# Performance work log

Hardware: AMD Instinct MI355X
Metric: run time of the kernel (lower is better)

The kernel has to match this reference:

```python
import jax, jax.numpy as jnp
import numpy as np

T_SCALES = [0.0, 0.25, 0.5, 0.75, 1.0]  # ODEblock time_scales; Euler step per consecutive pair
NUM_ZEROS = 10
BETA = 0.6  # defined in ODEFunc but unused in its forward


def _odefunc(x, x0, adj, alpha, w, d, w2, d2):
    # x: [B, N, T, Fa]; adj: [N, N]; alpha: [N]; w: [Fa, Fa]; d: [Fa]; w2: [T, T]; d2: [T]
    a = jax.nn.sigmoid(alpha)[None, :, None, None]              # [1, N, 1, 1]
    xa = jnp.einsum('ij,kjln->kiln', adj, x)                    # adjacency propagation over nodes
    dc = jnp.clip(d, 0.0, 1.0)
    W = (w * dc) @ w.T                                          # [Fa, Fa]
    # NOTE: faithful to torch source: 'ijkl,mn->ijkm' has NO shared contraction
    # index => xw = (sum_l x) outer (sum_n W) — reproduced exactly.
    xw = jnp.einsum('ijkl,mn->ijkm', x, W)
    d2c = jnp.clip(d2, 0.0, 1.0)
    W2 = (w2 * d2c) @ w2.T                                      # [T, T]
    xw2 = jnp.einsum('ijkl,kn->ijnl', x, W2)                    # temporal mixing
    # f = alpha/2*xa - x + xw - x + xw2 - x + x0
    return a * 0.5 * xa - 3.0 * x + xw + xw2 + x0


def setup_inputs() -> dict:
    key = jax.random.key(0)
    k1, k2 = jax.random.split(key)
    B, N, T, F = 32, 512, 24, 64
    Fa = F + NUM_ZEROS
    x = jax.random.normal(k1, (B, N, T, F), dtype=jnp.float32)
    adj = jax.random.uniform(k2, (N, N), dtype=jnp.float32) / N  # normalized dense adjacency
    alpha = 0.8 * jnp.ones((N,), jnp.float32)                    # nn.Parameter init 0.8*ones
    w = jnp.eye(Fa, dtype=jnp.float32)                           # nn.Parameter init eye
    d = jnp.ones((Fa,), jnp.float32)                             # nn.Parameter init ones
    w2 = jnp.eye(T, dtype=jnp.float32)
    d2 = jnp.ones((T,), jnp.float32)
    return {"x": x, "adj": adj, "alpha": alpha, "w": w, "d": d, "w2": w2, "d2": d2}


def reference(x, adj, alpha, w, d, w2, d2):
    B, N, T, F = x.shape
    if F == 64:
        x_aug = jnp.concatenate(
            [x, jnp.zeros((B, N, T, NUM_ZEROS), dtype=x.dtype)], axis=3)
    else:
        x_aug = x
    x0 = jax.lax.stop_gradient(x_aug)  # set_x0 uses clone().detach()
    # Euler odeint with two time points does one step: z = x + dt * f(x).
    # Original loop restarts from x_aug each iteration, so f is constant.
    f = _odefunc(x_aug, x0, adj, alpha, w, d, w2, d2)
    z = x_aug
    for i in range(len(T_SCALES) - 1):
        dt = T_SCALES[i + 1] - T_SCALES[i]
        z = x_aug + dt * f  # overwrites z each iteration, as in the torch code
    return jax.nn.relu(z)
```

## Files before the change

### kernel.cpp

```cpp
#include <hip/hip_runtime.h>
#include <hip/hip_fp16.h>
#include <cstdint>
#include <cstddef>

#define B_  32
#define N_  512
#define T_  24
#define F_  64
#define FA_ 74
#define NC  1536

typedef __attribute__((ext_vector_type(8))) _Float16 half8;
typedef __attribute__((ext_vector_type(8))) unsigned short ushort8;
typedef __attribute__((ext_vector_type(4))) float floatx4;

#define WS_ADJ 1536
#define WS_XT  132608
#define WS_S   12715520

#define AS1(p) ((const __attribute__((address_space(1))) void*)(p))
#define AS3(p) ((__attribute__((address_space(3))) void*)(p))

union h2u { _Float16 h; unsigned short u; };

__global__ __launch_bounds__(256) void prep_kernel(
    const float* __restrict__ x, const float* __restrict__ adj,
    const float* __restrict__ alpha, const float* __restrict__ w,
    const float* __restrict__ d, const float* __restrict__ w2,
    const float* __restrict__ d2, float* __restrict__ ws) {
  __shared__ float tile[64 * 65];
  __shared__ float cs[FA_];
  int bid = blockIdx.x;
  int tid = threadIdx.x;
  if (bid < 6144) {
    _Float16* xT = (_Float16*)(ws + WS_XT);
    float* Sp = ws + WS_S;
    int ct = bid % 24;
    int kt = (bid / 24) % 8;
    int b = bid / 192;
    int c0 = ct * 64;
    int k0 = kt * 64;
#pragma unroll
    for (int it = 0; it < 4; ++it) {
      int g = it * 256 + tid;
      int k = g >> 4, c4 = g & 15;
      float4 v = *(const float4*)&x[((size_t)(b * N_ + k0 + k)) * NC + c0 + c4 * 4];
      tile[k * 65 + c4 * 4 + 0] = v.x;
      tile[k * 65 + c4 * 4 + 1] = v.y;
      tile[k * 65 + c4 * 4 + 2] = v.z;
      tile[k * 65 + c4 * 4 + 3] = v.w;
    }
    __syncthreads();
    {
      int k = tid >> 2, q = tid & 3;
      float s = 0.f;
#pragma unroll
      for (int j = 0; j < 16; ++j) s += tile[k * 65 + q * 16 + j];
      s += __shfl_xor(s, 1, 64);
      s += __shfl_xor(s, 2, 64);
      if (q == 0) Sp[((size_t)b * T_ + ct) * N_ + k0 + k] = s;
    }
#pragma unroll
    for (int it = 0; it < 4; ++it) {
      int hh = it * 256 + tid;
      int c = hh >> 4, k4 = hh & 15;
      ushort4 u4; h2u cv;
      cv.h = (_Float16)tile[(k4 * 4 + 0) * 65 + c]; u4.x = cv.u;
      cv.h = (_Float16)tile[(k4 * 4 + 1) * 65 + c]; u4.y = cv.u;
      cv.h = (_Float16)tile[(k4 * 4 + 2) * 65 + c]; u4.z = cv.u;
      cv.h = (_Float16)tile[(k4 * 4 + 3) * 65 + c]; u4.w = cv.u;
      *(ushort4*)&xT[((size_t)b * NC + c0 + c) * 512 + k0 + k4 * 4] = u4;
    }
  } else if (bid < 6400) {
    _Float16* adjH = (_Float16*)(ws + WS_ADJ);
    int g = ((bid - 6144) * 256 + tid) * 4;
    int row = g >> 9;
    float sc = 0.125f / (1.f + __expf(-alpha[row]));
    float4 v = *(const float4*)&adj[g];
    ushort4 u4; h2u cv;
    cv.h = (_Float16)(sc * v.x); u4.x = cv.u;
    cv.h = (_Float16)(sc * v.y); u4.y = cv.u;
    cv.h = (_Float16)(sc * v.z); u4.z = cv.u;
    cv.h = (_Float16)(sc * v.w); u4.w = cv.u;
    *(ushort4*)&adjH[g] = u4;
  } else {
    if (tid < FA_) {
      float s = 0.f;
      for (int n = 0; n < FA_; ++n) s += w[n * FA_ + tid];
      cs[tid] = s;
    }
    __syncthreads();
    if (tid < FA_) {
      float s = 0.f;
      for (int p = 0; p < FA_; ++p) {
        float dc = fminf(fmaxf(d[p], 0.f), 1.f);
        s += w[tid * FA_ + p] * dc * cs[p];
      }
      ws[tid] = s;
    }
    for (int e = tid; e < T_ * T_; e += 256) {
      int a = e / T_, b = e % T_;
      float s = 0.f;
      for (int p = 0; p < T_; ++p) {
        float dc = fminf(fmaxf(d2[p], 0.f), 1.f);
        s += w2[a * T_ + p] * dc * w2[b * T_ + p];
      }
      ws[128 + e] = s;
    }
  }
}

__global__ __launch_bounds__(256) void gemm_kernel(
    const float* __restrict__ ws, const float* __restrict__ x,
    float* __restrict__ out) {
  const _Float16* adjH = (const _Float16*)(ws + WS_ADJ);
  const _Float16* xT   = (const _Float16*)(ws + WS_XT);
  const float* Sp      = ws + WS_S;

  __shared__ __align__(16) char smem[33792];
  _Float16* As = (_Float16*)smem;
  _Float16* Bs = (_Float16*)(smem + 16384);
  float* accS = (float*)smem;
  __shared__ float coefs[48];

  int raw = blockIdx.x;
  int nid = (raw & 7) * 192 + (raw >> 3);
  int iq = nid & 3;
  int rest = nid >> 2;
  int cb = rest % 12;
  int b = rest / 12;
  int i0 = iq * 128;
  int c0 = cb * 128;
  int t0 = cb * 2;

  int tid = threadIdx.x;
  int wave = tid >> 6, lane = tid & 63;
  int mw = (wave & 1) * 64, nw = (wave >> 1) * 64;
  int l15 = lane & 15, l4 = lane >> 4;

  if (tid < 48) {
    int tl = tid / 24, tp = tid - (tid / 24) * 24;
    float cf = 0.25f * ws[128 + (t0 + tl) * 24 + tp];
    if (tp == t0 + tl) cf += 0.5f;
    coefs[tid] = cf;
  }

  floatx4 acc[4][4];
#pragma unroll
  for (int mt = 0; mt < 4; ++mt)
#pragma unroll
    for (int nt = 0; nt < 4; ++nt) acc[mt][nt] = (floatx4){0.f, 0.f, 0.f, 0.f};

  const size_t bC = (size_t)b * NC;
  for (int k0 = 0; k0 < 512; k0 += 64) {
#pragma unroll
    for (int rep = 0; rep < 4; ++rep) {
      int chunk = rep * 256 + tid;
      int r = chunk >> 3;
      int s = chunk & 7;
      int ss = (s ^ (r & 7)) * 8;
      __builtin_amdgcn_global_load_lds(AS1(adjH + (size_t)(i0 + r) * 512 + k0 + ss),
                                       AS3(&As[chunk * 8]), 16, 0, 0);
      __builtin_amdgcn_global_load_lds(AS1(xT + (bC + c0 + r) * 512 + k0 + ss),
                                       AS3(&Bs[chunk * 8]), 16, 0, 0);
    }
    __syncthreads();
#pragma unroll
    for (int ks = 0; ks < 2; ++ks) {
      half8 af[4], bfv[4];
#pragma unroll
      for (int mt = 0; mt < 4; ++mt) {
        int row = mw + mt * 16 + l15;
        int slot = (ks * 4 + l4) ^ (row & 7);
        af[mt] = *(const half8*)&As[row * 64 + slot * 8];
      }
#pragma unroll
      for (int nt = 0; nt < 4; ++nt) {
        int row = nw + nt * 16 + l15;
        int slot = (ks * 4 + l4) ^ (row & 7);
        bfv[nt] = *(const half8*)&Bs[row * 64 + slot * 8];
      }
#pragma unroll
      for (int mt = 0; mt < 4; ++mt)
#pragma unroll
        for (int nt = 0; nt < 4; ++nt)
          acc[mt][nt] = __builtin_amdgcn_mfma_f32_16x16x32_f16(af[mt], bfv[nt], acc[mt][nt], 0, 0, 0);
    }
    __syncthreads();
  }

  const size_t bN = (size_t)b * N_;
  int f = tid & 63;
  int rj = tid >> 6;
  float rsWf = ws[f];
  float rsWa = (f < 10) ? ws[64 + f] : 0.f;
  const float* SpT = Sp + ((size_t)b * T_ + t0) * N_;
  for (int h = 0; h < 2; ++h) {
    if ((wave & 1) == h) {
#pragma unroll
      for (int mt = 0; mt < 4; ++mt)
#pragma unroll
        for (int nt = 0; nt < 4; ++nt)
#pragma unroll
          for (int r = 0; r < 4; ++r)
            accS[(mt * 16 + l4 * 4 + r) * 132 + nw + nt * 16 + l15] = acc[mt][nt][r];
    }
    __syncthreads();

#pragma unroll 2
    for (int jj = 0; jj < 16; ++jj) {
      int row = rj + 4 * jj;
      int grow = i0 + h * 64 + row;
      const float* xr = x + (bN + grow) * NC;
      float xv[24];
#pragma unroll
      for (int tp = 0; tp < 24; ++tp) xv[tp] = xr[tp * 64 + f];
      float s0 = SpT[grow];
      float s1 = SpT[N_ + grow];
      float tm0 = 0.f, tm1 = 0.f;
#pragma unroll
      for (int tp = 0; tp < 24; ++tp) {
        tm0 += coefs[tp] * xv[tp];
        tm1 += coefs[24 + tp] * xv[tp];
      }
      float v0 = accS[row * 132 + f]      + tm0 + 0.25f * s0 * rsWf;
      float v1 = accS[row * 132 + 64 + f] + tm1 + 0.25f * s1 * rsWf;
      size_t o = ((bN + grow) * T_ + t0) * FA_ + f;
      out[o] = fmaxf(v0, 0.f);
      out[o + FA_] = fmaxf(v1, 0.f);
      if (f < 10) {
        out[o + 64] = fmaxf(0.25f * s0 * rsWa, 0.f);
        out[o + FA_ + 64] = fmaxf(0.25f * s1 * rsWa, 0.f);
      }
    }
    __syncthreads();
  }
}

extern "C" void kernel_launch(void* const* d_in, const int* in_sizes, int n_in,
                              void* d_out, int out_size, void* d_ws, size_t ws_size,
                              hipStream_t stream) {
  const float* x     = (const float*)d_in[0];
  const float* adj   = (const float*)d_in[1];
  const float* alpha = (const float*)d_in[2];
  const float* w     = (const float*)d_in[3];
  const float* d     = (const float*)d_in[4];
  const float* w2    = (const float*)d_in[5];
  const float* d2    = (const float*)d_in[6];
  float* out = (float*)d_out;
  float* ws  = (float*)d_ws;

  hipLaunchKernelGGL(prep_kernel, dim3(6401), dim3(256), 0, stream,
                     x, adj, alpha, w, d, w2, d2, ws);
  hipLaunchKernelGGL(gemm_kernel, dim3(1536), dim3(256), 0, stream, ws, x, out);
}
```

Measured before the change: 325.2 us.

## Halve GEMM K-tile and LDS footprint, compute feature sums via wave shuffles

The GEMM kernel's K-step drops from 64 to 32, which halves the LDS staging buffers (about 33 KB down to about 17 KB), and the epilogue now writes accumulators back in four 32-row passes instead of two 64-row passes. The per-row feature sum is now taken from the already loaded x values with a wave-wide shuffle reduction rather than read from the precomputed Sp buffer. The aim is higher occupancy from less shared memory and fewer global reads of Sp in the epilogue. The cost is twice as many barriers per K sweep, less MFMA work between syncs, and extra shuffle and sync overhead in the epilogue. The prep kernel still computes and writes Sp, even though nothing reads it now.

```diff
diff --git a/kernel.cpp b/kernel.cpp
--- a/kernel.cpp
+++ b/kernel.cpp
@@ -115,11 +115,10 @@
     float* __restrict__ out) {
   const _Float16* adjH = (const _Float16*)(ws + WS_ADJ);
   const _Float16* xT   = (const _Float16*)(ws + WS_XT);
-  const float* Sp      = ws + WS_S;
-
-  __shared__ __align__(16) char smem[33792];
+
+  __shared__ __align__(16) char smem[16896];
   _Float16* As = (_Float16*)smem;
-  _Float16* Bs = (_Float16*)(smem + 16384);
+  _Float16* Bs = (_Float16*)(smem + 8192);
   float* accS = (float*)smem;
   __shared__ float coefs[48];
 
@@ -152,40 +151,37 @@
     for (int nt = 0; nt < 4; ++nt) acc[mt][nt] = (floatx4){0.f, 0.f, 0.f, 0.f};
 
   const size_t bC = (size_t)b * NC;
-  for (int k0 = 0; k0 < 512; k0 += 64) {
-#pragma unroll
-    for (int rep = 0; rep < 4; ++rep) {
+  for (int k0 = 0; k0 < 512; k0 += 32) {
+#pragma unroll
+    for (int rep = 0; rep < 2; ++rep) {
       int chunk = rep * 256 + tid;
-      int r = chunk >> 3;
-      int s = chunk & 7;
-      int ss = (s ^ (r & 7)) * 8;
+      int r = chunk >> 2;
+      int s = chunk & 3;
+      int ss = (s ^ (r & 3)) * 8;
       __builtin_amdgcn_global_load_lds(AS1(adjH + (size_t)(i0 + r) * 512 + k0 + ss),
                                        AS3(&As[chunk * 8]), 16, 0, 0);
       __builtin_amdgcn_global_load_lds(AS1(xT + (bC + c0 + r) * 512 + k0 + ss),
                                        AS3(&Bs[chunk * 8]), 16, 0, 0);
     }
     __syncthreads();
-#pragma unroll
-    for (int ks = 0; ks < 2; ++ks) {
-      half8 af[4], bfv[4];
-#pragma unroll
-      for (int mt = 0; mt < 4; ++mt) {
-        int row = mw + mt * 16 + l15;
-        int slot = (ks * 4 + l4) ^ (row & 7);
-        af[mt] = *(const half8*)&As[row * 64 + slot * 8];
-      }
-#pragma unroll
-      for (int nt = 0; nt < 4; ++nt) {
-        int row = nw + nt * 16 + l15;
-        int slot = (ks * 4 + l4) ^ (row & 7);
-        bfv[nt] = *(const half8*)&Bs[row * 64 + slot * 8];
-      }
-#pragma unroll
-      for (int mt = 0; mt < 4; ++mt)
-#pragma unroll
-        for (int nt = 0; nt < 4; ++nt)
-          acc[mt][nt] = __builtin_amdgcn_mfma_f32_16x16x32_f16(af[mt], bfv[nt], acc[mt][nt], 0, 0, 0);
-    }
+    half8 af[4], bfv[4];
+#pragma unroll
+    for (int mt = 0; mt < 4; ++mt) {
+      int row = mw + mt * 16 + l15;
+      int slot = l4 ^ (row & 3);
+      af[mt] = *(const half8*)&As[row * 32 + slot * 8];
+    }
+#pragma unroll
+    for (int nt = 0; nt < 4; ++nt) {
+      int row = nw + nt * 16 + l15;
+      int slot = l4 ^ (row & 3);
+      bfv[nt] = *(const half8*)&Bs[row * 32 + slot * 8];
+    }
+#pragma unroll
+    for (int mt = 0; mt < 4; ++mt)
+#pragma unroll
+      for (int nt = 0; nt < 4; ++nt)
+        acc[mt][nt] = __builtin_amdgcn_mfma_f32_16x16x32_f16(af[mt], bfv[nt], acc[mt][nt], 0, 0, 0);
     __syncthreads();
   }
 
@@ -194,37 +190,41 @@
   int rj = tid >> 6;
   float rsWf = ws[f];
   float rsWa = (f < 10) ? ws[64 + f] : 0.f;
-  const float* SpT = Sp + ((size_t)b * T_ + t0) * N_;
-  for (int h = 0; h < 2; ++h) {
-    if ((wave & 1) == h) {
-#pragma unroll
-      for (int mt = 0; mt < 4; ++mt)
+  for (int p = 0; p < 4; ++p) {
+    if ((wave & 1) == (p >> 1)) {
+      int mtb = (p & 1) * 2;
+#pragma unroll
+      for (int mt2 = 0; mt2 < 2; ++mt2)
 #pragma unroll
         for (int nt = 0; nt < 4; ++nt)
 #pragma unroll
           for (int r = 0; r < 4; ++r)
-            accS[(mt * 16 + l4 * 4 + r) * 132 + nw + nt * 16 + l15] = acc[mt][nt][r];
+            accS[(mt2 * 16 + l4 * 4 + r) * 132 + nw + nt * 16 + l15] = acc[mtb + mt2][nt][r];
     }
     __syncthreads();
 
 #pragma unroll 2
-    for (int jj = 0; jj < 16; ++jj) {
-      int row = rj + 4 * jj;
-      int grow = i0 + h * 64 + row;
+    for (int jj = 0; jj < 8; ++jj) {
+      int lr = rj + 4 * jj;
+      int grow = i0 + p * 32 + lr;
       const float* xr = x + (bN + grow) * NC;
       float xv[24];
 #pragma unroll
       for (int tp = 0; tp < 24; ++tp) xv[tp] = xr[tp * 64 + f];
-      float s0 = SpT[grow];
-      float s1 = SpT[N_ + grow];
+      float s0 = xv[t0], s1 = xv[t0 + 1];
+#pragma unroll
+      for (int off = 32; off >= 1; off >>= 1) {
+        s0 += __shfl_xor(s0, off, 64);
+        s1 += __shfl_xor(s1, off, 64);
+      }
       float tm0 = 0.f, tm1 = 0.f;
 #pragma unroll
       for (int tp = 0; tp < 24; ++tp) {
         tm0 += coefs[tp] * xv[tp];
         tm1 += coefs[24 + tp] * xv[tp];
       }
-      float v0 = accS[row * 132 + f]      + tm0 + 0.25f * s0 * rsWf;
-      float v1 = accS[row * 132 + 64 + f] + tm1 + 0.25f * s1 * rsWf;
+      float v0 = accS[lr * 132 + f]      + tm0 + 0.25f * s0 * rsWf;
+      float v1 = accS[lr * 132 + 64 + f] + tm1 + 0.25f * s1 * rsWf;
       size_t o = ((bN + grow) * T_ + t0) * FA_ + f;
       out[o] = fmaxf(v0, 0.f);
       out[o + FA_] = fmaxf(v1, 0.f);
```

Result: slower. 331.7 us (+2.0%).
